# Performance work log

Hardware: AMD Instinct MI355X
Metric: run time of the kernel (lower is better)

Reference implementation:

```python
import jax, jax.numpy as jnp
import numpy as np

B, S, D, H, DK, DV = 4, 1024, 1024, 16, 64, 64


def setup_inputs() -> dict:
    key = jax.random.key(0)
    ks = jax.random.split(key, 12)
    sc = 0.02
    return {
        "q": jax.random.normal(ks[0], (B, S, D), jnp.float32),
        "k": jax.random.normal(ks[1], (B, S, D), jnp.float32),
        "v": jax.random.normal(ks[2], (B, S, D), jnp.float32),
        "attn_mask": jax.random.randint(ks[3], (B, S, S), 0, 2).astype(bool),
        "Wq": jax.random.normal(ks[4], (D, H * DK), jnp.float32) * sc,
        "bq": jnp.zeros((H * DK,), jnp.float32),
        "Wk": jax.random.normal(ks[5], (D, H * DK), jnp.float32) * sc,
        "bk": jnp.zeros((H * DK,), jnp.float32),
        "Wv": jax.random.normal(ks[6], (D, H * DV), jnp.float32) * sc,
        "bv": jnp.zeros((H * DV,), jnp.float32),
        "Wo": jax.random.normal(ks[7], (H * DV, D), jnp.float32) * sc,
        "bo": jnp.zeros((D,), jnp.float32),
    }


def _layer_norm(x, eps=1e-5):
    # fresh nn.LayerNorm in forward => weight=1, bias=0
    mu = jnp.mean(x, axis=-1, keepdims=True)
    var = jnp.mean(jnp.square(x - mu), axis=-1, keepdims=True)
    return (x - mu) * jax.lax.rsqrt(var + eps)


def reference(q, k, v, attn_mask, Wq, bq, Wk, bk, Wv, bv, Wo, bo):
    residual = q
    qs = (q @ Wq + bq).reshape(B, S, H, DK).transpose(0, 2, 1, 3)  # [B,H,S,dk]
    ks = (k @ Wk + bk).reshape(B, S, H, DK).transpose(0, 2, 1, 3)
    vs = (v @ Wv + bv).reshape(B, S, H, DV).transpose(0, 2, 1, 3)
    scores = jnp.einsum('bhqd,bhkd->bhqk', qs, ks) / jnp.sqrt(jnp.float32(DK))
    scores = jnp.where(attn_mask[:, None, :, :], jnp.float32(-1e9), scores)
    attention = jax.nn.softmax(scores, axis=-1)  # [B,H,S,S]
    context = jnp.einsum('bhqk,bhkd->bhqd', attention, vs)
    concat = context.transpose(0, 2, 1, 3).reshape(B, S, H * DV)
    output = concat @ Wo + bo
    return _layer_norm(output + residual), attention
```

## Files before the change

kernel.cpp:

```cpp
#include <hip/hip_runtime.h>
#include <hip/hip_bf16.h>
#include <stdint.h>

#define B_    4
#define S_    1024
#define D_    1024
#define H_    16
#define NTOK  4096

typedef __bf16 bf16_t;
typedef bf16_t bf16x8 __attribute__((ext_vector_type(8)));
typedef bf16_t bf16x4 __attribute__((ext_vector_type(4)));
typedef float  f32x4  __attribute__((ext_vector_type(4)));

__device__ __forceinline__ f32x4 mfma16(bf16x8 a, bf16x8 b, f32x4 c) {
  return __builtin_amdgcn_mfma_f32_16x16x32_bf16(a, b, c, 0, 0, 0);
}
__device__ __forceinline__ void gload16(const void* g, void* l) {
  __builtin_amdgcn_global_load_lds((__attribute__((address_space(1))) uint32_t*)g,
                                   (__attribute__((address_space(3))) uint32_t*)l, 16, 0, 0);
}
__device__ __forceinline__ bf16_t to_bf(float x) { return (bf16_t)x; }

__global__ void cvt3_kernel(const float* __restrict__ q, const float* __restrict__ k,
                            const float* __restrict__ v, bf16_t* __restrict__ qb,
                            bf16_t* __restrict__ kb, bf16_t* __restrict__ vb) {
  int z = blockIdx.z;
  const float* src = (z == 0) ? q : ((z == 1) ? k : v);
  bf16_t* dst = (z == 0) ? qb : ((z == 1) ? kb : vb);
  int i = blockIdx.x * blockDim.x + threadIdx.x;
  f32x4 val = ((const f32x4*)src)[i];
  bf16x4 o = { to_bf(val[0]), to_bf(val[1]), to_bf(val[2]), to_bf(val[3]) };
  ((bf16x4*)dst)[i] = o;
}

__global__ void wT4_kernel(const float* __restrict__ Wq, const float* __restrict__ Wk,
                           const float* __restrict__ Wv, const float* __restrict__ Wo,
                           bf16_t* __restrict__ WqT, bf16_t* __restrict__ WkT,
                           bf16_t* __restrict__ WvT, bf16_t* __restrict__ WoT) {
  int z = blockIdx.z;
  const float* W = (z == 0) ? Wq : ((z == 1) ? Wk : ((z == 2) ? Wv : Wo));
  bf16_t* WT = (z == 0) ? WqT : ((z == 1) ? WkT : ((z == 2) ? WvT : WoT));
  __shared__ float t[32][33];
  int bx = blockIdx.x * 32, by = blockIdx.y * 32;
  int tx = threadIdx.x, ty = threadIdx.y;
#pragma unroll
  for (int i = 0; i < 4; i++) t[ty + 8 * i][tx] = W[(size_t)(by + ty + 8 * i) * 1024 + bx + tx];
  __syncthreads();
#pragma unroll
  for (int i = 0; i < 4; i++)
    WT[(size_t)(bx + ty + 8 * i) * 1024 + by + tx] = to_bf(t[tx][ty + 8 * i]);
}

__global__ void maskpack_kernel(const uint32_t* __restrict__ m, uint32_t* __restrict__ out) {
  int t = blockIdx.x * blockDim.x + threadIdx.x;
  const uint32_t* p = m + (size_t)t * 8;
  uint32_t r = 0;
#pragma unroll
  for (int j = 0; j < 8; j++) {
    uint32_t v = p[j];
    uint32_t nib = (v & 1u) | ((v >> 7) & 2u) | ((v >> 14) & 4u) | ((v >> 21) & 8u);
    r |= nib << (j * 4);
  }
  out[t] = r;
}

__device__ __forceinline__ void gemm128_core(const bf16_t* __restrict__ A,
                                             const bf16_t* __restrict__ Bm,
                                             int m0, int n0,
                                             bf16_t* As, bf16_t* Bs, f32x4 (&acc)[4][4]) {
  int tid = threadIdx.x, w = tid >> 6, lane = tid & 63, l16 = lane & 15, lg = lane >> 4;
  int wr = w >> 1, wc = w & 1;
  f32x4 zv = {0.f, 0.f, 0.f, 0.f};
#pragma unroll
  for (int r = 0; r < 4; r++)
#pragma unroll
    for (int c = 0; c < 4; c++) acc[r][c] = zv;

  for (int kt = 0; kt < 16; kt++) {
    int k0 = kt * 64;
#pragma unroll
    for (int j = 0; j < 4; j++) {
      int e = ((w * 4 + j) << 9) + (lane << 3);
      int row = e >> 6, col = e & 63;
      gload16(A + (size_t)(m0 + row) * 1024 + k0 + col, As + ((w * 4 + j) << 9));
      gload16(Bm + (size_t)(n0 + row) * 1024 + k0 + col, Bs + ((w * 4 + j) << 9));
    }
    __syncthreads();
#pragma unroll
    for (int kk = 0; kk < 2; kk++) {
      bf16x8 av[4], bv[4];
#pragma unroll
      for (int r = 0; r < 4; r++)
        av[r] = *(const bf16x8*)(As + (wr * 64 + r * 16 + l16) * 64 + kk * 32 + lg * 8);
#pragma unroll
      for (int c = 0; c < 4; c++)
        bv[c] = *(const bf16x8*)(Bs + (wc * 64 + c * 16 + l16) * 64 + kk * 32 + lg * 8);
#pragma unroll
      for (int r = 0; r < 4; r++)
#pragma unroll
        for (int c = 0; c < 4; c++) acc[r][c] = mfma16(av[r], bv[c], acc[r][c]);
    }
    __syncthreads();
  }
}

__global__ __launch_bounds__(256, 2) void qkv_gemm_kernel(
    const bf16_t* __restrict__ qb, const bf16_t* __restrict__ kb, const bf16_t* __restrict__ vb,
    const bf16_t* __restrict__ WqT, const bf16_t* __restrict__ WkT, const bf16_t* __restrict__ WvT,
    const float* __restrict__ bq, const float* __restrict__ bk, const float* __restrict__ bv,
    bf16_t* __restrict__ Qh, bf16_t* __restrict__ Kh, bf16_t* __restrict__ Vh) {
  __shared__ bf16_t As[128 * 64], Bs[128 * 64];
  int z = blockIdx.z;
  const bf16_t* A  = (z == 0) ? qb  : ((z == 1) ? kb  : vb);
  const bf16_t* Bm = (z == 0) ? WqT : ((z == 1) ? WkT : WvT);
  const float* bias = (z == 0) ? bq : ((z == 1) ? bk : bv);
  bf16_t* out = (z == 0) ? Qh : ((z == 1) ? Kh : Vh);
  int m0 = blockIdx.y * 128, n0 = blockIdx.x * 128;
  f32x4 acc[4][4];
  gemm128_core(A, Bm, m0, n0, As, Bs, acc);

  int tid = threadIdx.x, w = tid >> 6, lane = tid & 63, l16 = lane & 15, lg = lane >> 4;
  int wr = w >> 1, wc = w & 1;
#pragma unroll
  for (int c = 0; c < 4; c++) {
    int col = n0 + wc * 64 + c * 16 + l16;
    float bb = bias[col];
#pragma unroll
    for (int r = 0; r < 4; r++) {
#pragma unroll
      for (int i = 0; i < 4; i++) {
        int mrow = m0 + wr * 64 + r * 16 + lg * 4 + i;
        out[(size_t)mrow * 1024 + col] = to_bf(acc[r][c][i] + bb);
      }
    }
  }
}

__global__ void vT_kernel(const bf16_t* __restrict__ Vh, bf16_t* __restrict__ Vt) {
  __shared__ float t[64][65];
  int bh = blockIdx.z * 16 + blockIdx.y;
  int b = blockIdx.z, h = blockIdx.y;
  int s0 = blockIdx.x * 64;
  int tx = threadIdx.x & 63, ty = threadIdx.x >> 6;
  bf16_t* dst = Vt + (size_t)bh * 65536;
#pragma unroll
  for (int i = 0; i < 16; i++)
    t[ty + 4 * i][tx] = (float)Vh[(size_t)(b * 1024 + s0 + ty + 4 * i) * 1024 + h * 64 + tx];
  __syncthreads();
#pragma unroll
  for (int i = 0; i < 16; i++)
    dst[(size_t)(ty + 4 * i) * 1024 + s0 + tx] = to_bf(t[tx][ty + 4 * i]);
}

__global__ __launch_bounds__(256) void attn_kernel(
    const bf16_t* __restrict__ Qh, const bf16_t* __restrict__ Kh, const bf16_t* __restrict__ Vt,
    const uint32_t* __restrict__ mbits, float* __restrict__ attn_out, bf16_t* __restrict__ ctx) {
  __shared__ uint32_t mb[1024];
  __shared__ float redm[128], reds[128];

  int lin = blockIdx.x + 32 * (blockIdx.y + 16 * blockIdx.z);
  int xcd = lin & 7;
  int slot = lin >> 3;
  int bh = xcd * 8 + (slot >> 5);
  int q0 = (slot & 31) * 32;
  int b = bh >> 4, h = bh & 15;

  int tid = threadIdx.x, w = tid >> 6, lane = tid & 63, l16 = lane & 15, lg = lane >> 4;

  ((uint4*)mb)[tid] = ((const uint4*)(mbits + ((size_t)b * 1024 + q0) * 32))[tid];

  bf16x8 qa[2][2];
#pragma unroll
  for (int r = 0; r < 2; r++)
#pragma unroll
    for (int kk = 0; kk < 2; kk++)
      qa[r][kk] = *(const bf16x8*)(Qh + (size_t)(b * 1024 + q0 + r * 16 + l16) * 1024 +
                                   h * 64 + kk * 32 + lg * 8);

  f32x4 zv = {0.f, 0.f, 0.f, 0.f};
  f32x4 sc[2][16];
#pragma unroll
  for (int rt = 0; rt < 2; rt++)
#pragma unroll
    for (int c = 0; c < 16; c++) sc[rt][c] = zv;
  int kcol0 = w * 256;
#pragma unroll 4
  for (int c = 0; c < 16; c++) {
#pragma unroll
    for (int kk = 0; kk < 2; kk++) {
      bf16x8 kv = *(const bf16x8*)(Kh + (size_t)(b * 1024 + kcol0 + c * 16 + l16) * 1024 +
                                   h * 64 + kk * 32 + lg * 8);
      sc[0][c] = mfma16(qa[0][kk], kv, sc[0][c]);
      sc[1][c] = mfma16(qa[1][kk], kv, sc[1][c]);
    }
  }
  __syncthreads();

  float rmax[2][4], rsum[2][4], rinv[2][4];
#pragma unroll
  for (int rt = 0; rt < 2; rt++)
#pragma unroll
    for (int i = 0; i < 4; i++) rmax[rt][i] = -3e38f;
  const float scale = 0.125f;
#pragma unroll
  for (int rt = 0; rt < 2; rt++) {
#pragma unroll
    for (int j = 0; j < 8; j++) {
      uint32_t wd[4];
#pragma unroll
      for (int i = 0; i < 4; i++) wd[i] = mb[(rt * 16 + lg * 4 + i) * 32 + w * 8 + j];
#pragma unroll
      for (int hf = 0; hf < 2; hf++) {
        int c = j * 2 + hf;
#pragma unroll
        for (int i = 0; i < 4; i++) {
          float s = sc[rt][c][i] * scale;
          if ((wd[i] >> (l16 + hf * 16)) & 1u) s = -1e9f;
          sc[rt][c][i] = s;
          rmax[rt][i] = fmaxf(rmax[rt][i], s);
        }
      }
    }
  }
#pragma unroll
  for (int m = 1; m < 16; m <<= 1)
#pragma unroll
    for (int rt = 0; rt < 2; rt++)
#pragma unroll
      for (int i = 0; i < 4; i++) rmax[rt][i] = fmaxf(rmax[rt][i], __shfl_xor(rmax[rt][i], m));
  if (l16 == 0) {
#pragma unroll
    for (int rt = 0; rt < 2; rt++)
#pragma unroll
      for (int i = 0; i < 4; i++) redm[w * 32 + rt * 16 + lg * 4 + i] = rmax[rt][i];
  }
  __syncthreads();
#pragma unroll
  for (int rt = 0; rt < 2; rt++)
#pragma unroll
    for (int i = 0; i < 4; i++) {
      int row = rt * 16 + lg * 4 + i;
      rmax[rt][i] = fmaxf(fmaxf(redm[row], redm[32 + row]), fmaxf(redm[64 + row], redm[96 + row]));
      rsum[rt][i] = 0.f;
    }
#pragma unroll
  for (int rt = 0; rt < 2; rt++)
#pragma unroll
    for (int c = 0; c < 16; c++)
#pragma unroll
      for (int i = 0; i < 4; i++) {
        float p = __expf(sc[rt][c][i] - rmax[rt][i]);
        sc[rt][c][i] = p;
        rsum[rt][i] += p;
      }
#pragma unroll
  for (int m = 1; m < 16; m <<= 1)
#pragma unroll
    for (int rt = 0; rt < 2; rt++)
#pragma unroll
      for (int i = 0; i < 4; i++) rsum[rt][i] += __shfl_xor(rsum[rt][i], m);
  if (l16 == 0) {
#pragma unroll
    for (int rt = 0; rt < 2; rt++)
#pragma unroll
      for (int i = 0; i < 4; i++) reds[w * 32 + rt * 16 + lg * 4 + i] = rsum[rt][i];
  }
  __syncthreads();
#pragma unroll
  for (int rt = 0; rt < 2; rt++)
#pragma unroll
    for (int i = 0; i < 4; i++) {
      int row = rt * 16 + lg * 4 + i;
      float gs = reds[row] + reds[32 + row] + reds[64 + row] + reds[96 + row];
      rinv[rt][i] = 1.0f / gs;
    }

  float* ob = attn_out + ((size_t)bh * 1024 + q0) * 1024;
#pragma unroll
  for (int rt = 0; rt < 2; rt++)
#pragma unroll
    for (int c = 0; c < 16; c++) {
      int colk = kcol0 + c * 16 + l16;
#pragma unroll
      for (int i = 0; i < 4; i++) {
        int row = rt * 16 + lg * 4 + i;
        ob[(size_t)row * 1024 + colk] = sc[rt][c][i] * rinv[rt][i];
      }
    }
  asm volatile("s_waitcnt vmcnt(0)" ::: "memory");
  __syncthreads();

  f32x4 oacc0 = zv, oacc1 = zv;
  const bf16_t* Vb = Vt + ((size_t)bh * 64 + w * 16 + l16) * 1024 + lg * 8;
  const float* prow0 = ob + (size_t)l16 * 1024 + lg * 8;
  const float* prow1 = ob + (size_t)(16 + l16) * 1024 + lg * 8;
#pragma unroll 4
  for (int ks = 0; ks < 32; ks++) {
    bf16x8 vv = *(const bf16x8*)(Vb + ks * 32);
    f32x4 x0 = *(const f32x4*)(prow0 + ks * 32);
    f32x4 x1 = *(const f32x4*)(prow0 + ks * 32 + 4);
    f32x4 y0 = *(const f32x4*)(prow1 + ks * 32);
    f32x4 y1 = *(const f32x4*)(prow1 + ks * 32 + 4);
    bf16x8 a0 = { to_bf(x0[0]), to_bf(x0[1]), to_bf(x0[2]), to_bf(x0[3]),
                  to_bf(x1[0]), to_bf(x1[1]), to_bf(x1[2]), to_bf(x1[3]) };
    bf16x8 a1 = { to_bf(y0[0]), to_bf(y0[1]), to_bf(y0[2]), to_bf(y0[3]),
                  to_bf(y1[0]), to_bf(y1[1]), to_bf(y1[2]), to_bf(y1[3]) };
    oacc0 = mfma16(a0, vv, oacc0);
    oacc1 = mfma16(a1, vv, oacc1);
  }
#pragma unroll
  for (int i = 0; i < 4; i++) {
    ctx[(size_t)(b * 1024 + q0 + lg * 4 + i) * 1024 + h * 64 + w * 16 + l16] = to_bf(oacc0[i]);
    ctx[(size_t)(b * 1024 + q0 + 16 + lg * 4 + i) * 1024 + h * 64 + w * 16 + l16] = to_bf(oacc1[i]);
  }
}

__global__ __launch_bounds__(256, 2) void out_gemm_kernel(
    const bf16_t* __restrict__ ctx, const bf16_t* __restrict__ WoT,
    const float* __restrict__ bo, const float* __restrict__ resid, float* __restrict__ preLN) {
  __shared__ bf16_t As[128 * 64], Bs[128 * 64];
  int m0 = blockIdx.y * 128, n0 = blockIdx.x * 128;
  f32x4 acc[4][4];
  gemm128_core(ctx, WoT, m0, n0, As, Bs, acc);
  int tid = threadIdx.x, w = tid >> 6, lane = tid & 63, l16 = lane & 15, lg = lane >> 4;
  int wr = w >> 1, wc = w & 1;
#pragma unroll
  for (int c = 0; c < 4; c++) {
    int col = n0 + wc * 64 + c * 16 + l16;
    float bb = bo[col];
#pragma unroll
    for (int r = 0; r < 4; r++) {
#pragma unroll
      for (int i = 0; i < 4; i++) {
        int mrow = m0 + wr * 64 + r * 16 + lg * 4 + i;
        preLN[(size_t)mrow * 1024 + col] = acc[r][c][i] + bb + resid[(size_t)mrow * 1024 + col];
      }
    }
  }
}

__global__ void ln_kernel(const float* __restrict__ pre, float* __restrict__ out) {
  int row = blockIdx.x, tid = threadIdx.x;
  const f32x4 v = ((const f32x4*)(pre + (size_t)row * 1024))[tid];
  float s = v[0] + v[1] + v[2] + v[3];
  float s2 = v[0] * v[0] + v[1] * v[1] + v[2] * v[2] + v[3] * v[3];
#pragma unroll
  for (int m = 32; m > 0; m >>= 1) { s += __shfl_xor(s, m); s2 += __shfl_xor(s2, m); }
  __shared__ float rs[4], rs2[4];
  int w = tid >> 6;
  if ((tid & 63) == 0) { rs[w] = s; rs2[w] = s2; }
  __syncthreads();
  float S = rs[0] + rs[1] + rs[2] + rs[3];
  float S2 = rs2[0] + rs2[1] + rs2[2] + rs2[3];
  float mu = S * (1.f / 1024.f);
  float var = S2 * (1.f / 1024.f) - mu * mu;
  float rstd = rsqrtf(var + 1e-5f);
  f32x4 o = { (v[0] - mu) * rstd, (v[1] - mu) * rstd, (v[2] - mu) * rstd, (v[3] - mu) * rstd };
  ((f32x4*)(out + (size_t)row * 1024))[tid] = o;
}

extern "C" void kernel_launch(void* const* d_in, const int* in_sizes, int n_in,
                              void* d_out, int out_size, void* d_ws, size_t ws_size,
                              hipStream_t stream) {
  const float* q  = (const float*)d_in[0];
  const float* k  = (const float*)d_in[1];
  const float* v  = (const float*)d_in[2];
  const uint8_t* mask = (const uint8_t*)d_in[3];
  const float* Wq = (const float*)d_in[4];
  const float* bq = (const float*)d_in[5];
  const float* Wk = (const float*)d_in[6];
  const float* bk = (const float*)d_in[7];
  const float* Wv = (const float*)d_in[8];
  const float* bv = (const float*)d_in[9];
  const float* Wo = (const float*)d_in[10];
  const float* bo = (const float*)d_in[11];

  char* wsp = (char*)d_ws;
  size_t off = 0;
  auto carve = [&](size_t bytes) { void* p = wsp + off; off += (bytes + 255) & ~(size_t)255; return p; };
  bf16_t* qb  = (bf16_t*)carve((size_t)NTOK * 1024 * 2);
  bf16_t* kb  = (bf16_t*)carve((size_t)NTOK * 1024 * 2);
  bf16_t* vb  = (bf16_t*)carve((size_t)NTOK * 1024 * 2);
  bf16_t* WqT = (bf16_t*)carve((size_t)1024 * 1024 * 2);
  bf16_t* WkT = (bf16_t*)carve((size_t)1024 * 1024 * 2);
  bf16_t* WvT = (bf16_t*)carve((size_t)1024 * 1024 * 2);
  bf16_t* WoT = (bf16_t*)carve((size_t)1024 * 1024 * 2);
  bf16_t* Qh  = (bf16_t*)carve((size_t)NTOK * 1024 * 2);
  bf16_t* Kh  = (bf16_t*)carve((size_t)NTOK * 1024 * 2);
  bf16_t* Vh  = (bf16_t*)carve((size_t)NTOK * 1024 * 2);
  bf16_t* Vt  = (bf16_t*)carve((size_t)NTOK * 1024 * 2);
  bf16_t* ctx = (bf16_t*)carve((size_t)NTOK * 1024 * 2);
  uint32_t* mbits = (uint32_t*)carve((size_t)B_ * S_ * 32 * 4);
  float* preLN = (float*)carve((size_t)NTOK * 1024 * 4);
  (void)ws_size; (void)in_sizes; (void)n_in; (void)out_size;

  float* lnout = (float*)d_out;
  float* attn_out = (float*)d_out + (size_t)NTOK * 1024;

  cvt3_kernel<<<dim3(4096, 1, 3), 256, 0, stream>>>(q, k, v, qb, kb, vb);
  wT4_kernel<<<dim3(32, 32, 4), dim3(32, 8), 0, stream>>>(Wq, Wk, Wv, Wo, WqT, WkT, WvT, WoT);
  maskpack_kernel<<<512, 256, 0, stream>>>((const uint32_t*)mask, mbits);
  qkv_gemm_kernel<<<dim3(8, 32, 3), 256, 0, stream>>>(qb, kb, vb, WqT, WkT, WvT,
                                                      bq, bk, bv, Qh, Kh, Vh);
  vT_kernel<<<dim3(16, 16, 4), 256, 0, stream>>>(Vh, Vt);
  attn_kernel<<<dim3(32, 16, 4), 256, 0, stream>>>(Qh, Kh, Vt, mbits, attn_out, ctx);
  out_gemm_kernel<<<dim3(8, 32), 256, 0, stream>>>(ctx, WoT, bo, q, preLN);
  ln_kernel<<<4096, 256, 0, stream>>>(preLN, lnout);
}
```

Before: 885.7 us.

## Split P@V out of attention kernel into separate LDS-tiled GEMM kernel

The attention kernel no longer computes context itself. Previously it wrote normalized probabilities to global memory, waited for them, and read them back per wave with little reuse of V. A new pv_gemm kernel tiles 128 query rows by 64 head dims, stages the fp32 probabilities (converted to bf16) and Vt through LDS, and uses MFMA across 4 waves. This adds a kernel launch and re-reads the 256MB attention matrix from HBM/cache, in exchange for better tiling and shorter attention blocks.

After: 829.4 us. -6.4%, faster.

```diff
diff --git a/kernel.cpp b/kernel.cpp
--- a/kernel.cpp
+++ b/kernel.cpp
@@ -153,9 +153,9 @@
     dst[(size_t)(ty + 4 * i) * 1024 + s0 + tx] = to_bf(t[tx][ty + 4 * i]);
 }
 
-__global__ __launch_bounds__(256) void attn_kernel(
-    const bf16_t* __restrict__ Qh, const bf16_t* __restrict__ Kh, const bf16_t* __restrict__ Vt,
-    const uint32_t* __restrict__ mbits, float* __restrict__ attn_out, bf16_t* __restrict__ ctx) {
+__global__ __launch_bounds__(256) void attn_score_kernel(
+    const bf16_t* __restrict__ Qh, const bf16_t* __restrict__ Kh,
+    const uint32_t* __restrict__ mbits, float* __restrict__ attn_out) {
   __shared__ uint32_t mb[1024];
   __shared__ float redm[128], reds[128];
 
@@ -288,32 +288,64 @@
         ob[(size_t)row * 1024 + colk] = sc[rt][c][i] * rinv[rt][i];
       }
     }
-  asm volatile("s_waitcnt vmcnt(0)" ::: "memory");
-  __syncthreads();
-
-  f32x4 oacc0 = zv, oacc1 = zv;
-  const bf16_t* Vb = Vt + ((size_t)bh * 64 + w * 16 + l16) * 1024 + lg * 8;
-  const float* prow0 = ob + (size_t)l16 * 1024 + lg * 8;
-  const float* prow1 = ob + (size_t)(16 + l16) * 1024 + lg * 8;
-#pragma unroll 4
-  for (int ks = 0; ks < 32; ks++) {
-    bf16x8 vv = *(const bf16x8*)(Vb + ks * 32);
-    f32x4 x0 = *(const f32x4*)(prow0 + ks * 32);
-    f32x4 x1 = *(const f32x4*)(prow0 + ks * 32 + 4);
-    f32x4 y0 = *(const f32x4*)(prow1 + ks * 32);
-    f32x4 y1 = *(const f32x4*)(prow1 + ks * 32 + 4);
-    bf16x8 a0 = { to_bf(x0[0]), to_bf(x0[1]), to_bf(x0[2]), to_bf(x0[3]),
-                  to_bf(x1[0]), to_bf(x1[1]), to_bf(x1[2]), to_bf(x1[3]) };
-    bf16x8 a1 = { to_bf(y0[0]), to_bf(y0[1]), to_bf(y0[2]), to_bf(y0[3]),
-                  to_bf(y1[0]), to_bf(y1[1]), to_bf(y1[2]), to_bf(y1[3]) };
-    oacc0 = mfma16(a0, vv, oacc0);
-    oacc1 = mfma16(a1, vv, oacc1);
-  }
-#pragma unroll
-  for (int i = 0; i < 4; i++) {
-    ctx[(size_t)(b * 1024 + q0 + lg * 4 + i) * 1024 + h * 64 + w * 16 + l16] = to_bf(oacc0[i]);
-    ctx[(size_t)(b * 1024 + q0 + 16 + lg * 4 + i) * 1024 + h * 64 + w * 16 + l16] = to_bf(oacc1[i]);
-  }
+}
+
+__global__ __launch_bounds__(256, 4) void pv_gemm_kernel(
+    const float* __restrict__ attn, const bf16_t* __restrict__ Vt, bf16_t* __restrict__ ctx) {
+  constexpr int PSTRA = 40;
+  __shared__ bf16_t As[128 * PSTRA];
+  __shared__ bf16_t Bs[64 * PSTRA];
+  int bh = blockIdx.y;
+  int m0 = blockIdx.x * 128;
+  int b = bh >> 4, h = bh & 15;
+  const float* Ab = attn + ((size_t)bh * 1024 + m0) * 1024;
+  const bf16_t* Bb = Vt + (size_t)bh * 65536;
+  int tid = threadIdx.x, w = tid >> 6, lane = tid & 63, l16 = lane & 15, lg = lane >> 4;
+  int arow = tid >> 1, acol = (tid & 1) * 16;
+  int brow = tid >> 2, bcol = (tid & 3) * 8;
+  f32x4 zv = {0.f, 0.f, 0.f, 0.f};
+  f32x4 acc[2][4];
+#pragma unroll
+  for (int r = 0; r < 2; r++)
+#pragma unroll
+    for (int c = 0; c < 4; c++) acc[r][c] = zv;
+
+  for (int kt = 0; kt < 32; kt++) {
+    int k0 = kt * 32;
+    f32x4 a0 = *(const f32x4*)(Ab + (size_t)arow * 1024 + k0 + acol);
+    f32x4 a1 = *(const f32x4*)(Ab + (size_t)arow * 1024 + k0 + acol + 4);
+    f32x4 a2 = *(const f32x4*)(Ab + (size_t)arow * 1024 + k0 + acol + 8);
+    f32x4 a3 = *(const f32x4*)(Ab + (size_t)arow * 1024 + k0 + acol + 12);
+    bf16x8 p0 = { to_bf(a0[0]), to_bf(a0[1]), to_bf(a0[2]), to_bf(a0[3]),
+                  to_bf(a1[0]), to_bf(a1[1]), to_bf(a1[2]), to_bf(a1[3]) };
+    bf16x8 p1 = { to_bf(a2[0]), to_bf(a2[1]), to_bf(a2[2]), to_bf(a2[3]),
+                  to_bf(a3[0]), to_bf(a3[1]), to_bf(a3[2]), to_bf(a3[3]) };
+    *(bf16x8*)(As + arow * PSTRA + acol) = p0;
+    *(bf16x8*)(As + arow * PSTRA + acol + 8) = p1;
+    *(bf16x8*)(Bs + brow * PSTRA + bcol) = *(const bf16x8*)(Bb + (size_t)brow * 1024 + k0 + bcol);
+    __syncthreads();
+    bf16x8 av[2], bv[4];
+#pragma unroll
+    for (int r = 0; r < 2; r++)
+      av[r] = *(const bf16x8*)(As + (w * 32 + r * 16 + l16) * PSTRA + lg * 8);
+#pragma unroll
+    for (int c = 0; c < 4; c++)
+      bv[c] = *(const bf16x8*)(Bs + (c * 16 + l16) * PSTRA + lg * 8);
+#pragma unroll
+    for (int r = 0; r < 2; r++)
+#pragma unroll
+      for (int c = 0; c < 4; c++) acc[r][c] = mfma16(av[r], bv[c], acc[r][c]);
+    __syncthreads();
+  }
+#pragma unroll
+  for (int r = 0; r < 2; r++)
+#pragma unroll
+    for (int c = 0; c < 4; c++)
+#pragma unroll
+      for (int i = 0; i < 4; i++) {
+        int row = m0 + w * 32 + r * 16 + lg * 4 + i;
+        ctx[(size_t)(b * 1024 + row) * 1024 + h * 64 + c * 16 + l16] = to_bf(acc[r][c][i]);
+      }
 }
 
 __global__ __launch_bounds__(256, 2) void out_gemm_kernel(
@@ -404,7 +436,8 @@
   qkv_gemm_kernel<<<dim3(8, 32, 3), 256, 0, stream>>>(qb, kb, vb, WqT, WkT, WvT,
                                                       bq, bk, bv, Qh, Kh, Vh);
   vT_kernel<<<dim3(16, 16, 4), 256, 0, stream>>>(Vh, Vt);
-  attn_kernel<<<dim3(32, 16, 4), 256, 0, stream>>>(Qh, Kh, Vt, mbits, attn_out, ctx);
+  attn_score_kernel<<<dim3(32, 16, 4), 256, 0, stream>>>(Qh, Kh, mbits, attn_out);
+  pv_gemm_kernel<<<dim3(8, 64), 256, 0, stream>>>(attn_out, Vt, ctx);
   out_gemm_kernel<<<dim3(8, 32), 256, 0, stream>>>(ctx, WoT, bo, q, preLN);
   ln_kernel<<<4096, 256, 0, stream>>>(preLN, lnout);
 }
```
